# Optimization experiments

Measured on AMD Instinct MI355X. Metric: run time of the kernel, lower is better.

Reference implementation:

```python
import jax, jax.numpy as jnp
import numpy as np
from math import comb

N_DERIV = 4          # num_derivatives
ODE_DIM = 512        # ode_dimension
K = ODE_DIM * (N_DERIV + 1)


def _build_system(n, d):
    # system_matrices_1d: A_1d = flip(pascal), Q_1d = flip(hilbert), chol(Q_1d)
    x = np.arange(n + 1)
    B = np.array([[comb(i, j) for j in range(n + 1)] for i in range(n + 1)], dtype=np.float64)
    A1 = B[::-1, ::-1]                                  # flip both axes
    Hil = 1.0 / (x[:, None] + x[None, :] + 1.0)
    Q1 = Hil[::-1, ::-1]
    L1 = np.linalg.cholesky(Q1)
    a = np.kron(np.eye(d), A1)
    q = np.kron(np.eye(d), L1)
    return jnp.asarray(a, jnp.float32), jnp.asarray(q, jnp.float32)


def _qr_r(x):
    # sqrtm_to_cholesky: upper-triangular factor from reduced QR
    return jnp.linalg.qr(x)[1]


def setup_inputs() -> dict:
    key = jax.random.key(0)
    k1, k2, k3, k4, k5 = jax.random.split(key, 5)
    a, q_sqrtm_lower = _build_system(N_DERIV, ODE_DIM)
    m0 = jax.random.normal(k1, (K,), dtype=jnp.float32)
    l0 = jnp.tril(jax.random.normal(k2, (K, K), dtype=jnp.float32) * 0.05)
    H = jax.random.normal(k3, (ODE_DIM, K), dtype=jnp.float32) * 0.1
    bias = jax.random.normal(k4, (ODE_DIM,), dtype=jnp.float32)
    dt = jax.random.uniform(k5, (1,), dtype=jnp.float32, minval=0.05, maxval=0.15)
    return {"m0": m0, "l0": l0, "H": H, "bias": bias, "dt": dt,
            "a": a, "q_sqrtm_lower": q_sqrtm_lower}


def reference(m0, l0, H, bias, dt, a, q_sqrtm_lower):
    d = H.shape[0]
    k = m0.shape[0]
    n1 = k // d                       # num_derivatives + 1
    # --- assemble_preconditioner ---
    powers = jnp.arange(n1 - 1, -1, -1, dtype=m0.dtype)
    scales = jnp.exp(jax.lax.lgamma(powers + 1.0))
    pw = powers + 0.5
    adt = jnp.abs(dt[0])
    p = jnp.tile(adt ** pw / scales, d)          # (k,)
    p_inv = jnp.tile(adt ** (-pw) * scales, d)   # (k,)
    # --- extrapolate_mean ---
    m0_p = p_inv * m0
    m_ext_p = a @ m0_p
    m_ext = p * m_ext_p
    # EK-style linearized observation residual
    m_obs = H @ m_ext - bias                     # (d,)
    # --- estimate_error ---
    l_obs_ns_e = H @ (p_inv[:, None] * q_sqrtm_lower)            # (d,k)
    l_obs_raw = _qr_r(l_obs_ns_e.T).T                            # lower (d,d)
    res_white = jax.scipy.linalg.solve_triangular(l_obs_raw.T, m_obs, lower=False)
    diffusion = jnp.sqrt(jnp.dot(res_white, res_white) / res_white.size)
    error = diffusion * jnp.sqrt(jnp.einsum('nj,nj->n', l_obs_raw, l_obs_raw))
    # --- complete_extrapolation (sum_of_sqrtm_factors) ---
    R1 = (a @ (p_inv[:, None] * l0)).T           # (k,k)
    R2 = (diffusion * q_sqrtm_lower).T           # (k,k)
    l_ext_p = _qr_r(jnp.vstack([R1, R2])).T      # lower (k,k)
    l_ext = p[:, None] * l_ext_p
    # --- final_correction ---
    l_obs_ns = H @ l_ext                         # (d,k)
    l_obs = _qr_r(l_obs_ns.T).T                  # lower (d,d)
    crosscov = l_ext @ l_obs_ns.T                # (k,d)
    gain = jax.scipy.linalg.cho_solve((l_obs, True), crosscov.T).T  # (k,d)
    m_cor = m_ext - gain @ m_obs
    l_cor = l_ext - gain @ l_obs_ns
    u = jnp.reshape(m_cor, (-1, d), order='F')[0]  # derivative-0 block
    return m_cor, l_cor, u, error, diffusion
```

## Files before the change

kernel.cpp:

```cpp
#include <hip/hip_runtime.h>
#include <math.h>

#define KDIM 2560
#define DDIM 512
#define NB 64

#define QM 2560
#define QM2 1024
#define QN 512
#define PW 16
#define QACT 528

#define OUT_LCOR 2560
#define OUT_U    6556160
#define OUT_ERR  6556672
#define OUT_DIFF 6557184


__global__ void k_setup(const float* dt, double* scal){
  if (threadIdx.x==0 && blockIdx.x==0){
    double adt = fabs((double)dt[0]);
    const double scales[5] = {24.0,6.0,2.0,1.0,1.0};
    for (int i=0;i<5;i++){
      double pw = (double)(4-i)+0.5;
      scal[i]   = pow(adt, pw)/scales[i];
      scal[5+i] = pow(adt,-pw)*scales[i];
    }
  }
}

__global__ __launch_bounds__(256) void k_mext_mobs(const float* a, const float* m0, const float* H,
                                                   const float* bias, const double* scal,
                                                   double* mext, double* mobs){
  __shared__ double me[KDIM];
  __shared__ double red[256];
  double pp[5], pv[5];
  #pragma unroll
  for (int i=0;i<5;i++){ pp[i]=scal[i]; pv[i]=scal[5+i]; }
  int tid=threadIdx.x;
  for (int r=tid; r<KDIM; r+=256){
    int j=r/5, i=r%5;
    const float* arow = a + (size_t)r*KDIM + 5*j;
    const float* m0b  = m0 + 5*j;
    double acc=0;
    #pragma unroll
    for (int l=0;l<5;l++) acc += (double)arow[l]*pv[l]*(double)m0b[l];
    me[r] = pp[i]*acc;
  }
  __syncthreads();
  if (blockIdx.x==0) for (int r=tid;r<KDIM;r+=256) mext[r]=me[r];
  int b = blockIdx.x;
  const float* Hr = H + (size_t)b*KDIM;
  double acc=0;
  for (int c=tid;c<KDIM;c+=256) acc += (double)Hr[c]*me[c];
  red[tid]=acc; __syncthreads();
  for (int s=128;s>0;s>>=1){ if (tid<s) red[tid]+=red[tid+s]; __syncthreads(); }
  if (tid==0) mobs[b] = red[0] - (double)bias[b];
}

__global__ void k_A2(const float* H, const float* q, const double* scal,
                     double* Atop, double* Abot){
  int idx = blockIdx.x*blockDim.x+threadIdx.x;
  if (idx >= QN*QM) return;
  double pv[5];
  #pragma unroll
  for (int t=0;t<5;t++) pv[t]=scal[5+t];
  int j = idx / QM;
  int i = idx % QM;
  int bi = i/5;
  double acc=0;
  #pragma unroll
  for (int t=0;t<5;t++)
    acc += (double)H[(size_t)j*QM + 5*bi+t]*pv[t]*(double)q[(size_t)(5*bi+t)*QM + i];
  if (i < 512) Atop[(size_t)j*QM2 + i] = acc;
  else         Abot[(size_t)j*2048 + (i-512)] = acc;
}

__global__ void k_copyB(const double* Gbot, double* AQ){
  int idx = blockIdx.x*blockDim.x+threadIdx.x;
  if (idx >= 512*512) return;
  int c = idx/512, rr = idx%512;
  AQ[(size_t)c*QM2 + 512 + rr] = (rr<=c) ? Gbot[(size_t)c*512 + rr] : 0.0;
}

__global__ __launch_bounds__(576) void qr_step(double* A, double* vhead, double* Tbufs, int p){
  int col0 = p*PW;
  int tid=threadIdx.x, wid=tid>>6, lane=tid&63;

  if (blockIdx.x > 0){
    int pc0 = col0 - PW;
    const double* T = Tbufs + (size_t)(p-1)*PW*PW;
    int cc = col0 + PW + ((int)blockIdx.x - 1);
    int m = QM2 - pc0; if (m>QACT) m=QACT;
    __shared__ double redu[9][PW];
    __shared__ double yshu[PW];
    __shared__ double wshu[PW];
    int lr = tid;
    double a = (lr<m)? A[(size_t)cc*QM2 + pc0 + lr] : 0.0;
    double vv[PW];
    #pragma unroll
    for (int j=0;j<PW;j++){
      double vj=0.0;
      if (lr<m){
        if (lr>j)       vj=A[(size_t)(pc0+j)*QM2 + pc0 + lr];
        else if (lr==j) vj=vhead[pc0+j];
      }
      vv[j]=vj;
    }
    #pragma unroll
    for (int j=0;j<PW;j++){
      double d=vv[j]*a;
      #pragma unroll
      for (int o=32;o>0;o>>=1) d+=__shfl_down(d,o);
      if (lane==0) redu[wid][j]=d;
    }
    __syncthreads();
    if (tid<PW){
      double y=0;
      #pragma unroll
      for (int t=0;t<9;t++) y+=redu[t][tid];
      yshu[tid]=y;
    }
    __syncthreads();
    if (tid<PW){
      double s=0;
      for (int t=0;t<=tid;t++) s+=T[t*PW+tid]*yshu[t];
      wshu[tid]=s;
    }
    __syncthreads();
    if (lr<m){
      double s=0;
      #pragma unroll
      for (int j=0;j<PW;j++) s+=vv[j]*wshu[j];
      A[(size_t)cc*QM2 + pc0 + lr]=a-s;
    }
    return;
  }

  __shared__ double redw[9][PW];
  __shared__ double rednorm[9];
  __shared__ double sh[3];
  __shared__ double wsh[PW];
  __shared__ double alphas[PW], betas[PW];
  __shared__ double VtVs[PW][PW];
  __shared__ double Tsh[PW][PW];
  __shared__ double redP[9][PW*PW];
  __shared__ double ysh2[PW][PW];
  __shared__ double wsh2[PW][PW];

  int m = QM2 - col0; if (m>QACT) m=QACT;
  bool on = tid < m;
  double x[PW];

  if (p>0){
    int pc0 = col0 - PW;
    const double* T = Tbufs + (size_t)(p-1)*PW*PW;
    int mp = QM2 - pc0; if (mp>QACT) mp=QACT;
    bool gA = on;
    bool gB = (tid>=560);
    int rowA = col0 + tid;
    int kB   = tid - 560;
    double vv[PW];
    #pragma unroll
    for (int j=0;j<PW;j++){
      double vj=0.0;
      if (gA){
        if (tid + PW < mp) vj = A[(size_t)(pc0+j)*QM2 + rowA];
      } else if (gB){
        if (kB>j)       vj=A[(size_t)(pc0+j)*QM2 + pc0 + kB];
        else if (kB==j) vj=vhead[pc0+j];
      }
      vv[j]=vj;
    }
    #pragma unroll
    for (int c=0;c<PW;c++){
      double a=0.0;
      if (gA)      a = A[(size_t)(col0+c)*QM2 + rowA];
      else if (gB) a = A[(size_t)(col0+c)*QM2 + pc0 + kB];
      x[c]=a;
    }
    #pragma unroll
    for (int c=0;c<PW;c++){
      #pragma unroll
      for (int j=0;j<PW;j++){
        double d=vv[j]*x[c];
        #pragma unroll
        for (int o=32;o>0;o>>=1) d+=__shfl_down(d,o);
        if (lane==0) redP[wid][c*PW+j]=d;
      }
    }
    __syncthreads();
    if (tid<PW*PW){
      double y=0;
      #pragma unroll
      for (int t=0;t<9;t++) y+=redP[t][tid];
      ysh2[tid>>4][tid&15]=y;
    }
    __syncthreads();
    if (tid<PW*PW){
      int c=tid>>4, jj=tid&15;
      double s=0;
      for (int t=0;t<=jj;t++) s+=T[t*PW+jj]*ysh2[c][t];
      wsh2[c][jj]=s;
    }
    __syncthreads();
    #pragma unroll
    for (int c=0;c<PW;c++){
      double s=0;
      #pragma unroll
      for (int j=0;j<PW;j++) s+=vv[j]*wsh2[c][j];
      x[c]-=s;
    }
    if (gB){
      #pragma unroll
      for (int c=0;c<PW;c++) A[(size_t)(col0+c)*QM2 + pc0 + kB] = x[c];
    }
    if (!on){
      #pragma unroll
      for (int c=0;c<PW;c++) x[c]=0.0;
    }
    __syncthreads();
  } else {
    #pragma unroll
    for (int j=0;j<PW;j++)
      x[j] = on ? A[(size_t)(col0+j)*QM2 + col0 + tid] : 0.0;
  }

  #pragma unroll
  for (int j=0;j<PW;j++){
    double v0 = (tid>=j && on)? x[j] : 0.0;
    double ps = v0*v0;
    #pragma unroll
    for (int o=32;o>0;o>>=1) ps += __shfl_down(ps,o);
    if (lane==0) rednorm[wid]=ps;
    if (tid==j) sh[0]=x[j];
    __syncthreads();
    if (tid==0){
      double s0=0;
      for (int t=0;t<9;t++) s0+=rednorm[t];
      double x1=sh[0];
      double nrm=sqrt(s0);
      double alpha=(x1>=0.0)?-nrm:nrm;
      double v1=x1-alpha;
      double vtv=s0-2.0*alpha*x1+alpha*alpha;
      double b=(vtv>0.0)?2.0/vtv:0.0;
      sh[1]=v1; sh[2]=b;
      alphas[j]=alpha; betas[j]=b;
      vhead[col0+j]=v1;
    }
    __syncthreads();
    if (tid==j) x[j]=sh[1];
    double b=sh[2];
    double v=(tid>=j && on)? x[j] : 0.0;
    #pragma unroll
    for (int t=0;t<PW;t++){
      if (t==j) continue;
      double pdot=v*x[t];
      #pragma unroll
      for (int o=32;o>0;o>>=1) pdot+=__shfl_down(pdot,o);
      if (lane==0) redw[wid][t]=pdot;
    }
    __syncthreads();
    if (tid<PW && tid!=j){
      double tot=0;
      #pragma unroll
      for (int t2=0;t2<9;t2++) tot+=redw[t2][tid];
      if (tid>j) wsh[tid]=b*tot;
      else       VtVs[tid][j]=tot;
    }
    __syncthreads();
    if (v!=0.0){
      #pragma unroll
      for (int t=j+1;t<PW;t++) x[t]-=wsh[t]*v;
    }
  }
  __syncthreads();
  if (tid<PW){
    int i=tid;
    Tsh[i][i]=betas[i];
    for (int j2=i+1;j2<PW;j2++){
      double z=0;
      for (int t=i;t<j2;t++) z+=Tsh[i][t]*VtVs[t][j2];
      Tsh[i][j2]=-betas[j2]*z;
    }
  }
  __syncthreads();
  for (int e=tid;e<PW*PW;e+=576){
    int i=e/PW, j2=e%PW;
    Tbufs[(size_t)p*PW*PW + e] = (j2>=i)? Tsh[i][j2] : 0.0;
  }
  if (on){
    #pragma unroll
    for (int j=0;j<PW;j++)
      A[(size_t)(col0+j)*QM2 + col0 + tid] = (tid==j)? alphas[j] : x[j];
  }
}

__global__ __launch_bounds__(512) void k_rpost(const double* Aq, const double* mobs,
                                               double* scal, float* out){
  __shared__ double b[DDIM];
  __shared__ double xs[DDIM];
  __shared__ double D[NB][NB+1];
  __shared__ double red[DDIM];
  __shared__ double g1sh[DDIM];
  int tid=threadIdx.x;
  {
    double s=0;
    for (int r=0;r<=tid;r++){ double v=Aq[(size_t)tid*QM2 + r]; s+=v*v; }
    g1sh[tid]=s;
  }
  b[tid]=mobs[tid];
  __syncthreads();
  for (int p=7;p>=0;p--){
    int b0=p*NB;
    for (int e=tid;e<NB*NB;e+=512){ int i=e&63, j2=e>>6; D[i][j2]=Aq[(size_t)(b0+j2)*QM2 + b0+i]; }
    __syncthreads();
    if (tid<64){
      double bi=b[b0+tid];
      for (int k=NB-1;k>=0;k--){
        double bk=__shfl(bi,k);
        double xk=bk/D[k][k];
        if (tid<k) bi-=D[tid][k]*xk;
        if (tid==k) bi=xk;
      }
      xs[b0+tid]=bi;
    }
    __syncthreads();
    if (tid<b0){
      double s=0;
      #pragma unroll 8
      for (int j2=0;j2<NB;j2++) s+=Aq[(size_t)(b0+j2)*QM2 + tid]*xs[b0+j2];
      b[tid]-=s;
    }
    __syncthreads();
  }
  red[tid]=xs[tid]*xs[tid]; __syncthreads();
  for (int s=256;s>0;s>>=1){ if (tid<s) red[tid]+=red[tid+s]; __syncthreads(); }
  double diff=sqrt(red[0]/(double)DDIM);
  if (tid==0){ scal[10]=diff; out[OUT_DIFF]=(float)diff; }
  out[OUT_ERR+tid]=(float)(diff*sqrt(fmax(g1sh[tid],0.0)));
}

__global__ void k_X(const float* a, const float* l0, const double* scal, float* X){
  int idx=blockIdx.x*blockDim.x+threadIdx.x;
  if (idx>=KDIM*KDIM) return;
  double pv[5];
  #pragma unroll
  for (int t=0;t<5;t++) pv[t]=scal[5+t];
  int r=idx/KDIM, c=idx%KDIM;
  int j=r/5;
  const float* arow = a + (size_t)r*KDIM + 5*j;
  double acc=0;
  #pragma unroll
  for (int l=0;l<5;l++)
    acc += (double)arow[l]*pv[l]*(double)l0[(size_t)(5*j+l)*KDIM+c];
  X[idx]=(float)acc;
}

template<typename TA,int ATR,typename TB,int BTR,int MODE>
__global__ __launch_bounds__(256) void gemm64(const TA* __restrict__ A,int lda,
                                              const TB* __restrict__ B,int ldb,
                                              void* __restrict__ Cv,int ldc,
                                              int K,int kmode){
  __shared__ double As[16][65];
  __shared__ double Bs[16][65];
  int tid=threadIdx.x, tx=tid&15, ty=tid>>4;
  int n0=blockIdx.x*64, m0=blockIdx.y*64;
  int ks=0, ke=K;
  if (kmode==1) ks=n0;
  else if (kmode==2) ke=min(K,n0+64);
  else if (kmode==3) ke=min(K,m0+64);
  else if (kmode==4) ks=m0;
  double acc[4][4]={};
  for (int k0=ks;k0<ke;k0+=16){
    if (ATR){
      for (int e=tid;e<16*64;e+=256){int k=e>>6,mm=e&63; As[k][mm]=(double)A[(size_t)(k0+k)*lda+m0+mm];}
    } else {
      for (int e=tid;e<64*16;e+=256){int mm=e>>4,k=e&15; As[k][mm]=(double)A[(size_t)(m0+mm)*lda+k0+k];}
    }
    if (BTR){
      for (int e=tid;e<64*16;e+=256){int nn=e>>4,k=e&15; Bs[k][nn]=(double)B[(size_t)(n0+nn)*ldb+k0+k];}
    } else {
      for (int e=tid;e<16*64;e+=256){int k=e>>6,nn=e&63; Bs[k][nn]=(double)B[(size_t)(k0+k)*ldb+n0+nn];}
    }
    __syncthreads();
    #pragma unroll
    for (int t=0;t<16;t++){
      double av[4],bv[4];
      #pragma unroll
      for (int i=0;i<4;i++){av[i]=As[t][ty+16*i];bv[i]=Bs[t][tx+16*i];}
      #pragma unroll
      for (int i=0;i<4;i++)
        #pragma unroll
        for (int j=0;j<4;j++) acc[i][j]+=av[i]*bv[j];
    }
    __syncthreads();
  }
  #pragma unroll
  for (int i=0;i<4;i++){
    #pragma unroll
    for (int j=0;j<4;j++){
      size_t idx=(size_t)(m0+ty+16*i)*ldc+n0+tx+16*j;
      if (MODE==0) ((double*)Cv)[idx]=acc[i][j];
      else if (MODE==1) ((double*)Cv)[idx]-=acc[i][j];
      else ((float*)Cv)[idx]=(float)acc[i][j];
    }
  }
}

__global__ __launch_bounds__(256) void syrk_lower(const float* __restrict__ X, const float* __restrict__ q,
                                                  const double* __restrict__ scal,
                                                  double* __restrict__ G, int n){
  int t = blockIdx.x;
  int u = (int)((sqrtf(8.0f*(float)t+1.0f)+1.0f)*0.5f);
  while ((u*(u-1))/2 > t) u--;
  while ((u*(u+1))/2 <= t) u++;
  int s = (KDIM/64) - u;
  int r = s + (t - (u*(u-1))/2);
  int S0=s*64, R0=r*64;
  __shared__ double As[16][65];
  __shared__ double Bs[16][65];
  int tid=threadIdx.x, tx=tid&15, ty=tid>>4;
  int kend=min(n, S0+80);
  double acc[4][4]={};
  for (int k0=0;k0<kend;k0+=16){
    for (int e=tid;e<64*16;e+=256){int mm=e>>4,k=e&15; As[k][mm]=(double)X[(size_t)(R0+mm)*n+k0+k];}
    for (int e=tid;e<64*16;e+=256){int nn=e>>4,k=e&15; Bs[k][nn]=(double)X[(size_t)(S0+nn)*n+k0+k];}
    __syncthreads();
    #pragma unroll
    for (int t2=0;t2<16;t2++){
      double av[4],bv[4];
      #pragma unroll
      for (int i=0;i<4;i++){av[i]=As[t2][ty+16*i];bv[i]=Bs[t2][tx+16*i];}
      #pragma unroll
      for (int i=0;i<4;i++)
        #pragma unroll
        for (int j=0;j<4;j++) acc[i][j]+=av[i]*bv[j];
    }
    __syncthreads();
  }
  double dd = scal[10]*scal[10];
  #pragma unroll
  for (int i=0;i<4;i++)
    #pragma unroll
    for (int j=0;j<4;j++){
      int rr=R0+ty+16*i, c=S0+tx+16*j;
      double v=acc[i][j];
      if (c<=rr && (rr/5)==(c/5)){
        double qq=0;
        #pragma unroll
        for (int k=0;k<5;k++) qq += (double)q[(size_t)(rr%5)*KDIM+k]*(double)q[(size_t)(c%5)*KDIM+k];
        v += dd*qq;
      }
      G[(size_t)rr*n+c]=v;
    }
}

__global__ __launch_bounds__(256) void chol_diag(double* A, int n, int k0){
  __shared__ double P[NB][NB+1];
  int tid=threadIdx.x;
  for (int e=tid;e<NB*NB;e+=256){int r=e>>6,c=e&63;P[r][c]=A[(size_t)(k0+r)*n+k0+c];}
  int tx=tid&15, ty=tid>>4;
  __syncthreads();
  for (int j=0;j<NB;j++){
    double pj=P[j][j];
    __syncthreads();
    double rpj=1.0/sqrt(fmax(pj,1e-280));
    if (tid>j && tid<NB) P[tid][j]*=rpj;
    if (tid==j) P[j][j]=sqrt(fmax(pj,1e-280));
    __syncthreads();
    #pragma unroll
    for (int a2=0;a2<4;a2++){
      int r=ty+16*a2;
      double lrj=P[r][j];
      #pragma unroll
      for (int b2=0;b2<4;b2++){
        int c=tx+16*b2;
        if (r>j && c>j && c<=r) P[r][c]-=lrj*P[c][j];
      }
    }
    __syncthreads();
  }
  for (int e=tid;e<NB*NB;e+=256){int r=e>>6,c=e&63;A[(size_t)(k0+r)*n+k0+c]=P[r][c];}
}

__global__ __launch_bounds__(256) void chol_trsm(double* A,int n,int k0){
  __shared__ double Ls[NB][NB+1];
  __shared__ double St[NB][NB+1];
  __shared__ double rec[NB];
  int tid=threadIdx.x;
  for (int e=tid;e<NB*NB;e+=256){int r=e>>6,c=e&63;Ls[r][c]=A[(size_t)(k0+r)*n+k0+c];}
  __syncthreads();
  if (tid<NB) rec[tid]=1.0/Ls[tid][tid];
  int base=k0+NB+blockIdx.x*256;
  int myrow=base+tid;
  int mychunk=tid>>6, lrow=tid&63;
  double ar[NB];
  for (int ch=0;ch<4;ch++){
    int r0=base+ch*64;
    for (int e=tid;e<NB*NB;e+=256){
      int r=e>>6,c=e&63;
      if (r0+r<n) St[r][c]=A[(size_t)(r0+r)*n+k0+c];
    }
    __syncthreads();
    if (mychunk==ch && myrow<n){
      #pragma unroll
      for (int c=0;c<NB;c++) ar[c]=St[lrow][c];
    }
    __syncthreads();
  }
  if (myrow<n){
    #pragma unroll
    for (int j=0;j<NB;j++){
      double s=ar[j];
      #pragma unroll
      for (int t=0;t<j;t++) s-=ar[t]*Ls[j][t];
      ar[j]=s*rec[j];
    }
  }
  for (int ch=0;ch<4;ch++){
    int r0=base+ch*64;
    if (mychunk==ch && myrow<n){
      #pragma unroll
      for (int c=0;c<NB;c++) St[lrow][c]=ar[c];
    }
    __syncthreads();
    for (int e=tid;e<NB*NB;e+=256){
      int r=e>>6,c=e&63;
      if (r0+r<n) A[(size_t)(r0+r)*n+k0+c]=St[r][c];
    }
    __syncthreads();
  }
}

__global__ __launch_bounds__(256) void chol_syrk_fd(double* A,int n,int k0,int fuse){
  int ts0=k0+NB;
  int t=blockIdx.x;
  int r=(int)((sqrtf(8.0f*(float)t+1.0f)-1.0f)*0.5f);
  while ((r*(r+1))/2 > t) r--;
  while (((r+1)*(r+2))/2 <= t) r++;
  int s=t-(r*(r+1))/2;
  int S0=ts0+s*64, R0=ts0+r*64;
  __shared__ double As[16][65];
  __shared__ double Bs[16][65];
  __shared__ double P[NB][NB+1];
  int tid=threadIdx.x, tx=tid&15, ty=tid>>4;
  double acc[4][4]={};
  for (int k0i=0;k0i<NB;k0i+=16){
    for (int e=tid;e<64*16;e+=256){int mm=e>>4,k=e&15; As[k][mm]=A[(size_t)(R0+mm)*n+k0+k0i+k];}
    for (int e=tid;e<64*16;e+=256){int nn=e>>4,k=e&15; Bs[k][nn]=A[(size_t)(S0+nn)*n+k0+k0i+k];}
    __syncthreads();
    #pragma unroll
    for (int tt=0;tt<16;tt++){
      double av[4],bv[4];
      #pragma unroll
      for (int i=0;i<4;i++){av[i]=As[tt][ty+16*i];bv[i]=Bs[tt][tx+16*i];}
      #pragma unroll
      for (int i=0;i<4;i++)
        #pragma unroll
        for (int j=0;j<4;j++) acc[i][j]+=av[i]*bv[j];
    }
    __syncthreads();
  }
  if (t!=0 || !fuse){
    #pragma unroll
    for (int i=0;i<4;i++)
      #pragma unroll
      for (int j=0;j<4;j++)
        A[(size_t)(R0+ty+16*i)*n+S0+tx+16*j]-=acc[i][j];
    return;
  }
  #pragma unroll
  for (int i=0;i<4;i++)
    #pragma unroll
    for (int j=0;j<4;j++)
      P[ty+16*i][tx+16*j] = A[(size_t)(R0+ty+16*i)*n+S0+tx+16*j] - acc[i][j];
  __syncthreads();
  for (int j=0;j<NB;j++){
    double pj=P[j][j];
    __syncthreads();
    double rpj=1.0/sqrt(fmax(pj,1e-280));
    if (tid>j && tid<NB) P[tid][j]*=rpj;
    if (tid==j) P[j][j]=sqrt(fmax(pj,1e-280));
    __syncthreads();
    #pragma unroll
    for (int a2=0;a2<4;a2++){
      int r2=ty+16*a2;
      double lrj=P[r2][j];
      #pragma unroll
      for (int b2=0;b2<4;b2++){
        int c=tx+16*b2;
        if (r2>j && c>j && c<=r2) P[r2][c]-=lrj*P[c][j];
      }
    }
    __syncthreads();
  }
  for (int e=tid;e<NB*NB;e+=256){int r2=e>>6,c=e&63;A[(size_t)(ts0+r2)*n+ts0+c]=P[r2][c];}
}

__global__ void k_extract(const double* G2, const double* scal, float* lext){
  int idx=blockIdx.x*blockDim.x+threadIdx.x;
  if (idx>=KDIM*KDIM) return;
  int r=idx/KDIM, c=idx%KDIM;
  double v = (c<=r)? scal[r%5]*G2[idx] : 0.0;
  lext[idx]=(float)v;
}

__global__ __launch_bounds__(256) void trinv_diag(const double* S, double* Linv){
  __shared__ double Ls[NB][NB+1];
  __shared__ double Ti[NB][NB+1];
  int jb=blockIdx.x, tid=threadIdx.x;
  for (int e=tid; e<DDIM*NB; e+=256){
    int r=e/NB, c=e%NB;
    Linv[(size_t)r*DDIM + jb*NB + c]=0.0;
  }
  for (int e=tid;e<NB*NB;e+=256){int r=e>>6,c=e&63; Ls[r][c]=S[(size_t)(jb*NB+r)*DDIM + jb*NB+c];}
  __syncthreads();
  if (tid<NB){
    int c=tid;
    for (int r=c;r<NB;r++){
      double s=(r==c)?1.0:0.0;
      for (int t=c;t<r;t++) s-=Ls[r][t]*Ti[t][c];
      Ti[r][c]=s/Ls[r][r];
    }
    for (int r=0;r<c;r++) Ti[r][c]=0.0;
  }
  __syncthreads();
  for (int e=tid;e<NB*NB;e+=256){int r=e>>6,c=e&63; Linv[(size_t)(jb*NB+r)*DDIM + jb*NB+c]=Ti[r][c];}
}

__global__ __launch_bounds__(256) void trinv_step(const double* S, double* Linv, int d){
  __shared__ double As[16][65];
  __shared__ double Bs[16][65];
  __shared__ double Ps[NB][NB+1];
  int jb=blockIdx.x, ib=jb+d;
  int tid=threadIdx.x, tx=tid&15, ty=tid>>4;
  double acc[4][4]={};
  int kstart=jb*NB, kend=ib*NB;
  for (int k0=kstart;k0<kend;k0+=16){
    for (int e=tid;e<64*16;e+=256){int mm=e>>4,k=e&15; As[k][mm]=S[(size_t)(ib*NB+mm)*DDIM + k0+k];}
    for (int e=tid;e<16*64;e+=256){int k=e>>6,nn=e&63; Bs[k][nn]=Linv[(size_t)(k0+k)*DDIM + jb*NB+nn];}
    __syncthreads();
    #pragma unroll
    for (int t=0;t<16;t++){
      double av[4],bv[4];
      #pragma unroll
      for (int i=0;i<4;i++){av[i]=As[t][ty+16*i];bv[i]=Bs[t][tx+16*i];}
      #pragma unroll
      for (int i=0;i<4;i++)
        #pragma unroll
        for (int j=0;j<4;j++) acc[i][j]+=av[i]*bv[j];
    }
    __syncthreads();
  }
  #pragma unroll
  for (int i=0;i<4;i++)
    #pragma unroll
    for (int j=0;j<4;j++) Ps[ty+16*i][tx+16*j]=acc[i][j];
  double o[4][4]={};
  __syncthreads();
  for (int k0=0;k0<NB;k0+=16){
    for (int e=tid;e<64*16;e+=256){int mm=e>>4,k=e&15; As[k][mm]=Linv[(size_t)(ib*NB+mm)*DDIM + ib*NB+k0+k];}
    __syncthreads();
    #pragma unroll
    for (int t=0;t<16;t++){
      double av[4],bv[4];
      #pragma unroll
      for (int i=0;i<4;i++){av[i]=As[t][ty+16*i];bv[i]=Ps[k0+t][tx+16*i];}
      #pragma unroll
      for (int i=0;i<4;i++)
        #pragma unroll
        for (int j=0;j<4;j++) o[i][j]+=av[i]*bv[j];
    }
    __syncthreads();
  }
  #pragma unroll
  for (int i=0;i<4;i++)
    #pragma unroll
    for (int j=0;j<4;j++)
      Linv[(size_t)(ib*NB+ty+16*i)*DDIM + jb*NB+tx+16*j] = -o[i][j];
}

__global__ void k_mcor(const double* Z, const double* mobs, const double* mext, float* out){
  __shared__ double mo[DDIM];
  for (int s=threadIdx.x;s<DDIM;s+=256) mo[s]=mobs[s];
  __syncthreads();
  int r=blockIdx.x*256+threadIdx.x;
  if (r>=KDIM) return;
  double acc=0;
  for (int s=0;s<DDIM;s++) acc += Z[(size_t)s*KDIM+r]*mo[s];
  double mc = mext[r]-acc;
  out[r]=(float)mc;
  if (r%5==0) out[OUT_U + r/5]=(float)mc;
}

__global__ __launch_bounds__(256) void k_lcor(const double* __restrict__ Z, const float* __restrict__ lobs,
                                              const float* __restrict__ lext, float* __restrict__ out){
  __shared__ double As[16][65];
  __shared__ double Bs[16][65];
  int tid=threadIdx.x, tx=tid&15, ty=tid>>4;
  int n0=blockIdx.x*64, m0=blockIdx.y*64;
  double acc[4][4]={};
  for (int k0=0;k0<DDIM;k0+=16){
    for (int e=tid;e<16*64;e+=256){int k=e>>6,mm=e&63; As[k][mm]=Z[(size_t)(k0+k)*KDIM+m0+mm];}
    for (int e=tid;e<16*64;e+=256){int k=e>>6,nn=e&63; Bs[k][nn]=(double)lobs[(size_t)(k0+k)*KDIM+n0+nn];}
    __syncthreads();
    #pragma unroll
    for (int t=0;t<16;t++){
      double av[4],bv[4];
      #pragma unroll
      for (int i=0;i<4;i++){av[i]=As[t][ty+16*i];bv[i]=Bs[t][tx+16*i];}
      #pragma unroll
      for (int i=0;i<4;i++)
        #pragma unroll
        for (int j=0;j<4;j++) acc[i][j]+=av[i]*bv[j];
    }
    __syncthreads();
  }
  #pragma unroll
  for (int i=0;i<4;i++)
    #pragma unroll
    for (int j=0;j<4;j++){
      size_t idx=(size_t)(m0+ty+16*i)*KDIM+n0+tx+16*j;
      out[OUT_LCOR+idx]=(float)((double)lext[idx]-acc[i][j]);
    }
}

extern "C" void kernel_launch(void* const* d_in, const int* in_sizes, int n_in,
                              void* d_out, int out_size, void* d_ws, size_t ws_size,
                              hipStream_t stream) {
  const float* m0  = (const float*)d_in[0];
  const float* l0  = (const float*)d_in[1];
  const float* H   = (const float*)d_in[2];
  const float* bias= (const float*)d_in[3];
  const float* dt  = (const float*)d_in[4];
  const float* a   = (const float*)d_in[5];
  const float* q   = (const float*)d_in[6];
  float* out = (float*)d_out;

  char* w=(char*)d_ws;
  auto alloc=[&](size_t bytes)->char*{ char* p=w; w += ((bytes+255)/256)*256; return p; };
  double* scal  =(double*)alloc(16*8);
  double* mext  =(double*)alloc((size_t)KDIM*8);
  double* mobs  =(double*)alloc((size_t)DDIM*8);
  double* vheadA=(double*)alloc((size_t)QN*8);
  double* Tbufs =(double*)alloc((size_t)(QN/PW)*PW*PW*8);
  double* AQ    =(double*)alloc((size_t)QM2*QN*8);
  double* S     =(double*)alloc((size_t)DDIM*DDIM*8);
  double* G2    =(double*)alloc((size_t)KDIM*KDIM*8);
  float*  LOBS  =(float*) alloc((size_t)DDIM*KDIM*4);
  float*  X     =(float*) alloc((size_t)KDIM*KDIM*4);
  float*  LEXT  = X;
  double* Abot  = G2;
  double* Gbot  = Abot + (size_t)2048*512;
  double* Linv  = G2;
  double* C2    = Linv + (size_t)DDIM*DDIM;
  double* Y     = C2   + (size_t)DDIM*KDIM;
  double* Z     = Y    + (size_t)DDIM*KDIM;

  auto chol_full=[&](double* M, int n){
    chol_diag<<<1,256,0,stream>>>(M, n, 0);
    for (int k0=0;k0+NB<n;k0+=NB){
      int m = n-k0-NB;
      chol_trsm<<<(m+255)/256,256,0,stream>>>(M,n,k0);
      int T = m/64;
      chol_syrk_fd<<<T*(T+1)/2,256,0,stream>>>(M,n,k0,1);
    }
  };

  k_setup<<<1,1,0,stream>>>(dt, scal);
  k_mext_mobs<<<DDIM,256,0,stream>>>(a, m0, H, bias, scal, mext, mobs);

  k_A2<<<(QN*QM+255)/256,256,0,stream>>>(H, q, scal, AQ, Abot);
  gemm64<double,0,double,1,0><<<dim3(8,8),256,0,stream>>>(Abot,2048, Abot,2048, Gbot,512, 2048, 0);
  chol_full(Gbot, 512);
  k_copyB<<<(512*512+255)/256,256,0,stream>>>(Gbot, AQ);
  for (int p=0;p<QN/PW;p++){
    int nlz = QN - (p+1)*PW;
    int grid = 1 + ((p>0)? nlz : 0);
    qr_step<<<grid,576,0,stream>>>(AQ, vheadA, Tbufs, p);
  }
  k_rpost<<<1,512,0,stream>>>(AQ, mobs, scal, out);

  k_X<<<(KDIM*KDIM+255)/256,256,0,stream>>>(a, l0, scal, X);
  syrk_lower<<<(KDIM/64)*((KDIM/64)+1)/2,256,0,stream>>>(X, q, scal, G2, KDIM);
  chol_full(G2, KDIM);
  k_extract<<<(KDIM*KDIM+255)/256,256,0,stream>>>(G2, scal, LEXT);

  gemm64<float,0,float,0,2><<<dim3(KDIM/64,DDIM/64),256,0,stream>>>(H,KDIM, LEXT,KDIM, LOBS,KDIM, KDIM, 1);
  gemm64<float,0,float,1,0><<<dim3(DDIM/64,DDIM/64),256,0,stream>>>(LOBS,KDIM, LOBS,KDIM, S,DDIM, KDIM, 0);
  chol_full(S, DDIM);
  trinv_diag<<<8,256,0,stream>>>(S, Linv);
  for (int d=1;d<8;d++)
    trinv_step<<<8-d,256,0,stream>>>(S, Linv, d);
  gemm64<float,0,float,1,0><<<dim3(KDIM/64,DDIM/64),256,0,stream>>>(LOBS,KDIM, LEXT,KDIM, C2,KDIM, KDIM, 2);
  gemm64<double,0,double,0,0><<<dim3(KDIM/64,DDIM/64),256,0,stream>>>(Linv,DDIM, C2,KDIM, Y,KDIM, DDIM, 3);
  gemm64<double,1,double,0,0><<<dim3(KDIM/64,DDIM/64),256,0,stream>>>(Linv,DDIM, Y,KDIM, Z,KDIM, DDIM, 4);

  k_mcor<<<(KDIM+255)/256,256,0,stream>>>(Z, mobs, mext, out);
  k_lcor<<<dim3(KDIM/64,KDIM/64),256,0,stream>>>(Z, LOBS, LEXT, out);
}
```

Before: 15.73 ms.

## Fuse Cholesky panel solve into trailing update and shrink GEMM tiles

The separate per-panel TRSM kernel is merged into the trailing-update kernel. Each block re-solves the two row panels it needs in registers and feeds them straight into shared memory for the SYRK, which halves the kernel launches per panel step. Because the fused kernel never writes the solved panels back, a final chol_sweep kernel over all panels recomputes and stores them. Separately, the generic GEMM moves from 64x64 to 32x32 tiles to give small matrices more blocks, at the cost of less register reuse per thread and redundant TRSM work across blocks.

```diff
diff --git a/kernel.cpp b/kernel.cpp
--- a/kernel.cpp
+++ b/kernel.cpp
@@ -358,48 +358,48 @@
 }
 
 template<typename TA,int ATR,typename TB,int BTR,int MODE>
-__global__ __launch_bounds__(256) void gemm64(const TA* __restrict__ A,int lda,
+__global__ __launch_bounds__(256) void gemm32(const TA* __restrict__ A,int lda,
                                               const TB* __restrict__ B,int ldb,
                                               void* __restrict__ Cv,int ldc,
                                               int K,int kmode){
-  __shared__ double As[16][65];
-  __shared__ double Bs[16][65];
+  __shared__ double As[32][33];
+  __shared__ double Bs[32][33];
   int tid=threadIdx.x, tx=tid&15, ty=tid>>4;
-  int n0=blockIdx.x*64, m0=blockIdx.y*64;
+  int n0=blockIdx.x*32, m0=blockIdx.y*32;
   int ks=0, ke=K;
   if (kmode==1) ks=n0;
-  else if (kmode==2) ke=min(K,n0+64);
-  else if (kmode==3) ke=min(K,m0+64);
+  else if (kmode==2) ke=min(K,n0+32);
+  else if (kmode==3) ke=min(K,m0+32);
   else if (kmode==4) ks=m0;
-  double acc[4][4]={};
-  for (int k0=ks;k0<ke;k0+=16){
+  double acc[2][2]={};
+  for (int k0=ks;k0<ke;k0+=32){
     if (ATR){
-      for (int e=tid;e<16*64;e+=256){int k=e>>6,mm=e&63; As[k][mm]=(double)A[(size_t)(k0+k)*lda+m0+mm];}
+      for (int e=tid;e<32*32;e+=256){int k=e>>5,mm=e&31; As[k][mm]=(double)A[(size_t)(k0+k)*lda+m0+mm];}
     } else {
-      for (int e=tid;e<64*16;e+=256){int mm=e>>4,k=e&15; As[k][mm]=(double)A[(size_t)(m0+mm)*lda+k0+k];}
+      for (int e=tid;e<32*32;e+=256){int mm=e>>5,k=e&31; As[k][mm]=(double)A[(size_t)(m0+mm)*lda+k0+k];}
     }
     if (BTR){
-      for (int e=tid;e<64*16;e+=256){int nn=e>>4,k=e&15; Bs[k][nn]=(double)B[(size_t)(n0+nn)*ldb+k0+k];}
+      for (int e=tid;e<32*32;e+=256){int nn=e>>5,k=e&31; Bs[k][nn]=(double)B[(size_t)(n0+nn)*ldb+k0+k];}
     } else {
-      for (int e=tid;e<16*64;e+=256){int k=e>>6,nn=e&63; Bs[k][nn]=(double)B[(size_t)(k0+k)*ldb+n0+nn];}
-    }
-    __syncthreads();
-    #pragma unroll
-    for (int t=0;t<16;t++){
-      double av[4],bv[4];
-      #pragma unroll
-      for (int i=0;i<4;i++){av[i]=As[t][ty+16*i];bv[i]=Bs[t][tx+16*i];}
-      #pragma unroll
-      for (int i=0;i<4;i++)
+      for (int e=tid;e<32*32;e+=256){int k=e>>5,nn=e&31; Bs[k][nn]=(double)B[(size_t)(k0+k)*ldb+n0+nn];}
+    }
+    __syncthreads();
+    #pragma unroll
+    for (int t=0;t<32;t++){
+      double av[2],bv[2];
+      #pragma unroll
+      for (int i=0;i<2;i++){av[i]=As[t][ty+16*i];bv[i]=Bs[t][tx+16*i];}
+      #pragma unroll
+      for (int i=0;i<2;i++)
         #pragma unroll
-        for (int j=0;j<4;j++) acc[i][j]+=av[i]*bv[j];
-    }
-    __syncthreads();
-  }
-  #pragma unroll
-  for (int i=0;i<4;i++){
-    #pragma unroll
-    for (int j=0;j<4;j++){
+        for (int j=0;j<2;j++) acc[i][j]+=av[i]*bv[j];
+    }
+    __syncthreads();
+  }
+  #pragma unroll
+  for (int i=0;i<2;i++){
+    #pragma unroll
+    for (int j=0;j<2;j++){
       size_t idx=(size_t)(m0+ty+16*i)*ldc+n0+tx+16*j;
       if (MODE==0) ((double*)Cv)[idx]=acc[i][j];
       else if (MODE==1) ((double*)Cv)[idx]-=acc[i][j];
@@ -484,71 +484,52 @@
   for (int e=tid;e<NB*NB;e+=256){int r=e>>6,c=e&63;A[(size_t)(k0+r)*n+k0+c]=P[r][c];}
 }
 
-__global__ __launch_bounds__(256) void chol_trsm(double* A,int n,int k0){
+__global__ __launch_bounds__(256) void chol_step(double* __restrict__ A, int n, int k0){
   __shared__ double Ls[NB][NB+1];
-  __shared__ double St[NB][NB+1];
   __shared__ double rec[NB];
-  int tid=threadIdx.x;
-  for (int e=tid;e<NB*NB;e+=256){int r=e>>6,c=e&63;Ls[r][c]=A[(size_t)(k0+r)*n+k0+c];}
-  __syncthreads();
-  if (tid<NB) rec[tid]=1.0/Ls[tid][tid];
-  int base=k0+NB+blockIdx.x*256;
-  int myrow=base+tid;
-  int mychunk=tid>>6, lrow=tid&63;
-  double ar[NB];
-  for (int ch=0;ch<4;ch++){
-    int r0=base+ch*64;
-    for (int e=tid;e<NB*NB;e+=256){
-      int r=e>>6,c=e&63;
-      if (r0+r<n) St[r][c]=A[(size_t)(r0+r)*n+k0+c];
-    }
-    __syncthreads();
-    if (mychunk==ch && myrow<n){
-      #pragma unroll
-      for (int c=0;c<NB;c++) ar[c]=St[lrow][c];
-    }
-    __syncthreads();
-  }
-  if (myrow<n){
-    #pragma unroll
-    for (int j=0;j<NB;j++){
-      double s=ar[j];
-      #pragma unroll
-      for (int t=0;t<j;t++) s-=ar[t]*Ls[j][t];
-      ar[j]=s*rec[j];
-    }
-  }
-  for (int ch=0;ch<4;ch++){
-    int r0=base+ch*64;
-    if (mychunk==ch && myrow<n){
-      #pragma unroll
-      for (int c=0;c<NB;c++) St[lrow][c]=ar[c];
-    }
-    __syncthreads();
-    for (int e=tid;e<NB*NB;e+=256){
-      int r=e>>6,c=e&63;
-      if (r0+r<n) A[(size_t)(r0+r)*n+k0+c]=St[r][c];
-    }
-    __syncthreads();
-  }
-}
-
-__global__ __launch_bounds__(256) void chol_syrk_fd(double* A,int n,int k0,int fuse){
+  __shared__ double As[16][65];
+  __shared__ double Bs[16][65];
   int ts0=k0+NB;
   int t=blockIdx.x;
   int r=(int)((sqrtf(8.0f*(float)t+1.0f)-1.0f)*0.5f);
   while ((r*(r+1))/2 > t) r--;
   while (((r+1)*(r+2))/2 <= t) r++;
   int s=t-(r*(r+1))/2;
-  int S0=ts0+s*64, R0=ts0+r*64;
-  __shared__ double As[16][65];
-  __shared__ double Bs[16][65];
-  __shared__ double P[NB][NB+1];
+  int R0=ts0+r*NB, S0=ts0+s*NB;
   int tid=threadIdx.x, tx=tid&15, ty=tid>>4;
+  for (int e=tid;e<NB*NB;e+=256){int rr=e>>6,c=e&63;Ls[rr][c]=A[(size_t)(k0+rr)*n+k0+c];}
+  __syncthreads();
+  if (tid<NB) rec[tid]=1.0/Ls[tid][tid];
+  __syncthreads();
+  double ar[NB];
+  bool solver = (tid<64) || (tid<128 && s!=r);
+  int srow = (tid<64)? (R0+tid) : (S0+(tid-64));
+  if (solver){
+    #pragma unroll
+    for (int c=0;c<NB;c++) ar[c]=A[(size_t)srow*n + k0 + c];
+    #pragma unroll
+    for (int j=0;j<NB;j++){
+      double sv=ar[j];
+      #pragma unroll
+      for (int t2=0;t2<j;t2++) sv-=ar[t2]*Ls[j][t2];
+      ar[j]=sv*rec[j];
+    }
+  }
   double acc[4][4]={};
-  for (int k0i=0;k0i<NB;k0i+=16){
-    for (int e=tid;e<64*16;e+=256){int mm=e>>4,k=e&15; As[k][mm]=A[(size_t)(R0+mm)*n+k0+k0i+k];}
-    for (int e=tid;e<64*16;e+=256){int nn=e>>4,k=e&15; Bs[k][nn]=A[(size_t)(S0+nn)*n+k0+k0i+k];}
+  #pragma unroll
+  for (int c4=0;c4<4;c4++){
+    __syncthreads();
+    if (tid<64){
+      #pragma unroll
+      for (int k=0;k<16;k++) As[k][tid]=ar[c4*16+k];
+      if (s==r){
+        #pragma unroll
+        for (int k=0;k<16;k++) Bs[k][tid]=ar[c4*16+k];
+      }
+    } else if (tid<128 && s!=r){
+      #pragma unroll
+      for (int k=0;k<16;k++) Bs[k][tid-64]=ar[c4*16+k];
+    }
     __syncthreads();
     #pragma unroll
     for (int tt=0;tt<16;tt++){
@@ -560,9 +541,9 @@
         #pragma unroll
         for (int j=0;j<4;j++) acc[i][j]+=av[i]*bv[j];
     }
-    __syncthreads();
-  }
-  if (t!=0 || !fuse){
+  }
+  __syncthreads();
+  if (t!=0){
     #pragma unroll
     for (int i=0;i<4;i++)
       #pragma unroll
@@ -570,11 +551,12 @@
         A[(size_t)(R0+ty+16*i)*n+S0+tx+16*j]-=acc[i][j];
     return;
   }
+  double (*P)[NB+1] = Ls;
   #pragma unroll
   for (int i=0;i<4;i++)
     #pragma unroll
     for (int j=0;j<4;j++)
-      P[ty+16*i][tx+16*j] = A[(size_t)(R0+ty+16*i)*n+S0+tx+16*j] - acc[i][j];
+      P[ty+16*i][tx+16*j] = A[(size_t)(ts0+ty+16*i)*n+ts0+tx+16*j] - acc[i][j];
   __syncthreads();
   for (int j=0;j<NB;j++){
     double pj=P[j][j];
@@ -596,6 +578,56 @@
     __syncthreads();
   }
   for (int e=tid;e<NB*NB;e+=256){int r2=e>>6,c=e&63;A[(size_t)(ts0+r2)*n+ts0+c]=P[r2][c];}
+}
+
+__global__ __launch_bounds__(256) void chol_sweep(double* A, int n){
+  __shared__ double Ls[NB][NB+1];
+  __shared__ double St[NB][NB+1];
+  __shared__ double rec[NB];
+  int k0=blockIdx.y*NB;
+  int base=k0+NB+blockIdx.x*256;
+  if (base>=n) return;
+  int tid=threadIdx.x;
+  for (int e=tid;e<NB*NB;e+=256){int r2=e>>6,c=e&63;Ls[r2][c]=A[(size_t)(k0+r2)*n+k0+c];}
+  __syncthreads();
+  if (tid<NB) rec[tid]=1.0/Ls[tid][tid];
+  int myrow=base+tid, mychunk=tid>>6, lrow=tid&63;
+  double ar[NB];
+  for (int ch=0;ch<4;ch++){
+    int r0=base+ch*64;
+    for (int e=tid;e<NB*NB;e+=256){
+      int r2=e>>6,c=e&63;
+      if (r0+r2<n) St[r2][c]=A[(size_t)(r0+r2)*n+k0+c];
+    }
+    __syncthreads();
+    if (mychunk==ch && myrow<n){
+      #pragma unroll
+      for (int c=0;c<NB;c++) ar[c]=St[lrow][c];
+    }
+    __syncthreads();
+  }
+  if (myrow<n){
+    #pragma unroll
+    for (int j=0;j<NB;j++){
+      double s2=ar[j];
+      #pragma unroll
+      for (int t2=0;t2<j;t2++) s2-=ar[t2]*Ls[j][t2];
+      ar[j]=s2*rec[j];
+    }
+  }
+  for (int ch=0;ch<4;ch++){
+    int r0=base+ch*64;
+    if (mychunk==ch && myrow<n){
+      #pragma unroll
+      for (int c=0;c<NB;c++) St[lrow][c]=ar[c];
+    }
+    __syncthreads();
+    for (int e=tid;e<NB*NB;e+=256){
+      int r2=e>>6,c=e&63;
+      if (r0+r2<n) A[(size_t)(r0+r2)*n+k0+c]=St[r2][c];
+    }
+    __syncthreads();
+  }
 }
 
 __global__ void k_extract(const double* G2, const double* scal, float* lext){
@@ -761,18 +793,18 @@
   auto chol_full=[&](double* M, int n){
     chol_diag<<<1,256,0,stream>>>(M, n, 0);
     for (int k0=0;k0+NB<n;k0+=NB){
-      int m = n-k0-NB;
-      chol_trsm<<<(m+255)/256,256,0,stream>>>(M,n,k0);
-      int T = m/64;
-      chol_syrk_fd<<<T*(T+1)/2,256,0,stream>>>(M,n,k0,1);
-    }
+      int T = (n-k0-NB)/NB;
+      chol_step<<<T*(T+1)/2,256,0,stream>>>(M,n,k0);
+    }
+    dim3 g((n-NB+255)/256, n/NB-1);
+    chol_sweep<<<g,256,0,stream>>>(M,n);
   };
 
   k_setup<<<1,1,0,stream>>>(dt, scal);
   k_mext_mobs<<<DDIM,256,0,stream>>>(a, m0, H, bias, scal, mext, mobs);
 
   k_A2<<<(QN*QM+255)/256,256,0,stream>>>(H, q, scal, AQ, Abot);
-  gemm64<double,0,double,1,0><<<dim3(8,8),256,0,stream>>>(Abot,2048, Abot,2048, Gbot,512, 2048, 0);
+  gemm32<double,0,double,1,0><<<dim3(16,16),256,0,stream>>>(Abot,2048, Abot,2048, Gbot,512, 2048, 0);
   chol_full(Gbot, 512);
   k_copyB<<<(512*512+255)/256,256,0,stream>>>(Gbot, AQ);
   for (int p=0;p<QN/PW;p++){
@@ -787,15 +819,15 @@
   chol_full(G2, KDIM);
   k_extract<<<(KDIM*KDIM+255)/256,256,0,stream>>>(G2, scal, LEXT);
 
-  gemm64<float,0,float,0,2><<<dim3(KDIM/64,DDIM/64),256,0,stream>>>(H,KDIM, LEXT,KDIM, LOBS,KDIM, KDIM, 1);
-  gemm64<float,0,float,1,0><<<dim3(DDIM/64,DDIM/64),256,0,stream>>>(LOBS,KDIM, LOBS,KDIM, S,DDIM, KDIM, 0);
+  gemm32<float,0,float,0,2><<<dim3(KDIM/32,DDIM/32),256,0,stream>>>(H,KDIM, LEXT,KDIM, LOBS,KDIM, KDIM, 1);
+  gemm32<float,0,float,1,0><<<dim3(DDIM/32,DDIM/32),256,0,stream>>>(LOBS,KDIM, LOBS,KDIM, S,DDIM, KDIM, 0);
   chol_full(S, DDIM);
   trinv_diag<<<8,256,0,stream>>>(S, Linv);
   for (int d=1;d<8;d++)
     trinv_step<<<8-d,256,0,stream>>>(S, Linv, d);
-  gemm64<float,0,float,1,0><<<dim3(KDIM/64,DDIM/64),256,0,stream>>>(LOBS,KDIM, LEXT,KDIM, C2,KDIM, KDIM, 2);
-  gemm64<double,0,double,0,0><<<dim3(KDIM/64,DDIM/64),256,0,stream>>>(Linv,DDIM, C2,KDIM, Y,KDIM, DDIM, 3);
-  gemm64<double,1,double,0,0><<<dim3(KDIM/64,DDIM/64),256,0,stream>>>(Linv,DDIM, Y,KDIM, Z,KDIM, DDIM, 4);
+  gemm32<float,0,float,1,0><<<dim3(KDIM/32,DDIM/32),256,0,stream>>>(LOBS,KDIM, LEXT,KDIM, C2,KDIM, KDIM, 2);
+  gemm32<double,0,double,0,0><<<dim3(KDIM/32,DDIM/32),256,0,stream>>>(Linv,DDIM, C2,KDIM, Y,KDIM, DDIM, 3);
+  gemm32<double,1,double,0,0><<<dim3(KDIM/32,DDIM/32),256,0,stream>>>(Linv,DDIM, Y,KDIM, Z,KDIM, DDIM, 4);
 
   k_mcor<<<(KDIM+255)/256,256,0,stream>>>(Z, mobs, mext, out);
   k_lcor<<<dim3(KDIM/64,KDIM/64),256,0,stream>>>(Z, LOBS, LEXT, out);
```

Result: faster. 15.00 ms (-4.7%).
